# Kernel optimization log

Measured on AMD Instinct MI355X. Metric: run time of the kernel, lower is better.

Reference implementation:

```python
import jax, jax.numpy as jnp
import numpy as np

HEADS = 16
NU = 1
EPS = 1e-6


def dpfp(k):
    """Deterministic Parameter-Free Projection, normalized. k: [..., d_k] -> [..., 2*d_k*NU]."""
    x = jax.nn.relu(jnp.concatenate([k, -k], axis=-1))  # [..., 2*d_k]
    x_rolled = jnp.concatenate([jnp.roll(x, i, axis=-1) for i in range(1, NU + 1)], axis=-1)
    x_repeat = jnp.concatenate([x] * NU, axis=-1)
    phi = x_repeat * x_rolled
    return phi / (jnp.sum(phi, axis=-1, keepdims=True) + EPS)


def setup_inputs() -> dict:
    key = jax.random.key(0)
    ks = jax.random.split(key, 7)
    S, B, D, H = 4096, 4, 1024, HEADS
    scale = 0.02
    return {
        "x": jax.random.normal(ks[0], (S, B, D), dtype=jnp.float32),
        "Wq": jax.random.normal(ks[1], (D, D), dtype=jnp.float32) * scale,
        "Wk": jax.random.normal(ks[2], (D, D), dtype=jnp.float32) * scale,
        "Wv": jax.random.normal(ks[3], (D, D), dtype=jnp.float32) * scale,
        "Wb": jax.random.normal(ks[4], (D, H), dtype=jnp.float32) * scale,
        "Wo": jax.random.normal(ks[5], (D, D), dtype=jnp.float32) * scale,
        "bo": jnp.zeros((D,), dtype=jnp.float32),
    }


def reference(x, Wq, Wk, Wv, Wb, Wo, bo):
    S, B, D = x.shape
    H = HEADS
    dk = D // H
    d_dot = 2 * dk * NU

    # Projections: [S, B, H, d_k] (bias-free linears + head split)
    q = dpfp((x @ Wq).reshape(S, B, H, dk))   # [S, B, H, d_dot]
    k = dpfp((x @ Wk).reshape(S, B, H, dk))   # [S, B, H, d_dot]
    v = (x @ Wv).reshape(S, B, H, dk)          # [S, B, H, d_k]
    beta = jax.nn.sigmoid(x @ Wb).reshape(S, B, H, 1)  # [S, B, H, 1]

    W0 = jnp.zeros((B, H, dk, d_dot), dtype=x.dtype)  # fast-weight state

    def step(W, inputs):
        k_i, v_i, q_i, b_i = inputs  # [B,H,d_dot], [B,H,dk], [B,H,d_dot], [B,H,1]
        v_bar = jnp.einsum('bhvk,bhk->bhv', W, k_i)
        W = W + jnp.einsum('bhv,bhk->bhvk', b_i * (v_i - v_bar), k_i)
        y = jnp.einsum('bhvk,bhk->bhv', W, q_i)  # [B, H, dk]
        return W, y.reshape(B, H * dk)

    _, outputs = jax.lax.scan(step, W0, (k, v, q, beta))  # [S, B, D]
    return outputs @ Wo + bo
```

## Files before the change

kernel.cpp:

```cpp
#include <hip/hip_runtime.h>

#define S_LEN 4096
#define BATCH 4
#define NROWS 16384
#define DIM   1024
#define CHUNK 32
#define NCHUNK (S_LEN / CHUNK)

typedef __attribute__((ext_vector_type(8))) short short8;
typedef __attribute__((ext_vector_type(4))) float floatx4;
typedef _Float16 half_t;
typedef __attribute__((ext_vector_type(8))) _Float16 half8;

__device__ __forceinline__ float bf2f(short s) {
    union { unsigned int u; float f; } c;
    c.u = ((unsigned int)(unsigned short)s) << 16;
    return c.f;
}
__device__ __forceinline__ short f2bf(float f) {
    union { float f; unsigned int u; } c; c.f = f;
    unsigned int r = c.u + 0x7fffu + ((c.u >> 16) & 1u);
    return (short)(r >> 16);
}
__device__ __forceinline__ void split_bf16(float x, short& hi, short& lo) {
    short h = f2bf(x);
    hi = h;
    lo = f2bf(x - bf2f(h));
}

__device__ __forceinline__ float row16_allreduce(float x) {
    union fi { float f; int i; };
    fi a, b;
    a.f = x;
    b.i = __builtin_amdgcn_update_dpp(0, a.i, 0xB1,  0xF, 0xF, true); a.f += b.f;
    b.i = __builtin_amdgcn_update_dpp(0, a.i, 0x4E,  0xF, 0xF, true); a.f += b.f;
    b.i = __builtin_amdgcn_update_dpp(0, a.i, 0x124, 0xF, 0xF, true); a.f += b.f;
    b.i = __builtin_amdgcn_update_dpp(0, a.i, 0x128, 0xF, 0xF, true); a.f += b.f;
    return a.f;
}

__global__ __launch_bounds__(256) void transpose_k(const float* __restrict__ W,
                                                   float* __restrict__ Wt,
                                                   int K, int N) {
    int idx = blockIdx.x * 256 + threadIdx.x;
    if (idx >= N * K) return;
    int n = idx / K;
    int k = idx - n * K;
    Wt[idx] = W[k * N + n];
}

template <typename AT, int MODE>
__global__ __launch_bounds__(256) void gemm_bt(const AT* __restrict__ A,
                                               const float* __restrict__ Bt,
                                               void* __restrict__ Cout,
                                               const float* __restrict__ bias,
                                               int N, int K) {
    __shared__ __align__(16) short As_h[64][40], As_l[64][40];
    __shared__ __align__(16) short Bs_h[64][40], Bs_l[64][40];
    const int tid  = threadIdx.x;
    const int wave = tid >> 6, lane = tid & 63;
    const int row0 = blockIdx.x * 64, col0 = blockIdx.y * 64;
    const int lr = tid >> 2, lc = (tid & 3) * 8;
    const AT*    Ap = A  + (size_t)(row0 + lr) * K + lc;
    const float* Bp = Bt + (size_t)(col0 + lr) * K + lc;
    const int am = wave * 16 + (lane & 15);
    const int ak = (lane >> 4) * 8;
    floatx4 acc[4];
    #pragma unroll
    for (int t = 0; t < 4; ++t) acc[t] = (floatx4){0.f, 0.f, 0.f, 0.f};

    for (int k0 = 0; k0 < K; k0 += 32) {
        float av[8], bv[8];
        if constexpr (sizeof(AT) == 4) {
            floatx4 a0 = *(const floatx4*)(Ap + k0);
            floatx4 a1 = *(const floatx4*)(Ap + k0 + 4);
            #pragma unroll
            for (int j = 0; j < 4; ++j) { av[j] = a0[j]; av[4 + j] = a1[j]; }
        } else {
            half8 a = *(const half8*)(Ap + k0);
            #pragma unroll
            for (int j = 0; j < 8; ++j) av[j] = (float)a[j];
        }
        floatx4 b0 = *(const floatx4*)(Bp + k0);
        floatx4 b1 = *(const floatx4*)(Bp + k0 + 4);
        #pragma unroll
        for (int j = 0; j < 4; ++j) { bv[j] = b0[j]; bv[4 + j] = b1[j]; }

        short8 ah, al, bh, bl;
        #pragma unroll
        for (int j = 0; j < 8; ++j) {
            short h, l;
            split_bf16(av[j], h, l); ah[j] = h; al[j] = l;
            split_bf16(bv[j], h, l); bh[j] = h; bl[j] = l;
        }
        *(short8*)&As_h[lr][lc] = ah;
        *(short8*)&As_l[lr][lc] = al;
        *(short8*)&Bs_h[lr][lc] = bh;
        *(short8*)&Bs_l[lr][lc] = bl;
        __syncthreads();
        short8 afh = *(const short8*)&As_h[am][ak];
        short8 afl = *(const short8*)&As_l[am][ak];
        #pragma unroll
        for (int t = 0; t < 4; ++t) {
            short8 bfh = *(const short8*)&Bs_h[t * 16 + (lane & 15)][ak];
            short8 bfl = *(const short8*)&Bs_l[t * 16 + (lane & 15)][ak];
            acc[t] = __builtin_amdgcn_mfma_f32_16x16x32_bf16(afh, bfh, acc[t], 0, 0, 0);
            acc[t] = __builtin_amdgcn_mfma_f32_16x16x32_bf16(afh, bfl, acc[t], 0, 0, 0);
            acc[t] = __builtin_amdgcn_mfma_f32_16x16x32_bf16(afl, bfh, acc[t], 0, 0, 0);
        }
        __syncthreads();
    }
    const int crow = row0 + wave * 16 + (lane >> 4) * 4;
    const int ccol = lane & 15;
    #pragma unroll
    for (int t = 0; t < 4; ++t) {
        int col = col0 + t * 16 + ccol;
        #pragma unroll
        for (int r = 0; r < 4; ++r) {
            int row = crow + r;
            float v = acc[t][r];
            if (MODE == 0) {
                float b = bias ? bias[col] : 0.f;
                ((float*)Cout)[(size_t)row * N + col] = v + b;
            } else {
                ((half_t*)Cout)[(size_t)row * 2048 + (col >> 6) * 128 + (col & 63)] = (half_t)v;
            }
        }
    }
}

__global__ __launch_bounds__(256) void beta_kernel(const float* __restrict__ X,
                                                   const float* __restrict__ Wbt,
                                                   float* __restrict__ Beta) {
    int wid  = (blockIdx.x * 256 + threadIdx.x) >> 6;
    int lane = threadIdx.x & 63;
    if (wid >= NROWS) return;
    const float* xr = X + (size_t)wid * DIM + lane * 16;
    float xv[16];
    #pragma unroll
    for (int j = 0; j < 4; ++j) {
        floatx4 v = *(const floatx4*)(xr + j * 4);
        #pragma unroll
        for (int e = 0; e < 4; ++e) xv[j * 4 + e] = v[e];
    }
    #pragma unroll 1
    for (int h = 0; h < 16; ++h) {
        const float* wr = Wbt + h * DIM + lane * 16;
        float s = 0.f;
        #pragma unroll
        for (int j = 0; j < 4; ++j) {
            floatx4 v = *(const floatx4*)(wr + j * 4);
            #pragma unroll
            for (int e = 0; e < 4; ++e) s = fmaf(xv[j * 4 + e], v[e], s);
        }
        #pragma unroll
        for (int off = 32; off; off >>= 1) s += __shfl_xor(s, off);
        if (lane == 0) Beta[wid * 16 + h] = 1.f / (1.f + __expf(-s));
    }
}

__global__ __launch_bounds__(256) void dpfp_h(half_t* __restrict__ P) {
    int gw   = (blockIdx.x * 256 + threadIdx.x) >> 6;
    int lane = threadIdx.x & 63;
    half_t* base = P + (size_t)gw * 128;
    float p  = (float)base[lane];
    float pm = __shfl(p, (lane + 63) & 63);
    float rp  = fmaxf(p, 0.f),  rn  = fmaxf(-p, 0.f);
    float rpm = fmaxf(pm, 0.f), rnm = fmaxf(-pm, 0.f);
    float aprev = (lane == 0) ? rnm : rpm;
    float bprev = (lane == 0) ? rpm : rnm;
    float phi_a = rp * aprev;
    float phi_b = rn * bprev;
    float s = phi_a + phi_b;
    #pragma unroll
    for (int off = 32; off; off >>= 1) s += __shfl_xor(s, off);
    float inv = 1.f / (s + 1e-6f);
    base[lane]      = (half_t)(phi_a * inv);
    base[64 + lane] = (half_t)(phi_b * inv);
}


#define LOADSTEP(DK, DQ, STEP)                                              \
    {                                                                       \
        floatx4 _ka = *(const floatx4*)&Ks[bufi][STEP][tc * 8];             \
        floatx4 _kb = *(const floatx4*)&Ks[bufi][STEP][tc * 8 + 4];         \
        floatx4 _qa = *(const floatx4*)&Qs[bufi][STEP][tc * 8];             \
        floatx4 _qb = *(const floatx4*)&Qs[bufi][STEP][tc * 8 + 4];         \
        for (int _i = 0; _i < 4; ++_i) {                                    \
            DK[_i] = _ka[_i]; DK[4 + _i] = _kb[_i];                         \
            DQ[_i] = _qa[_i]; DQ[4 + _i] = _qb[_i];                         \
        }                                                                   \
    }

#define DOT8(RES, X, Y)                                                     \
    {                                                                       \
        float _s0 = X[0] * Y[0], _s1 = X[1] * Y[1];                         \
        _s0 = fmaf(X[2], Y[2], _s0); _s1 = fmaf(X[3], Y[3], _s1);           \
        _s0 = fmaf(X[4], Y[4], _s0); _s1 = fmaf(X[5], Y[5], _s1);           \
        _s0 = fmaf(X[6], Y[6], _s0); _s1 = fmaf(X[7], Y[7], _s1);           \
        RES = _s0 + _s1;                                                    \
    }

#define PAIR(CEK, CEQ, COK, COQ, CEV, CEB, COV, COB, CG,                    \
             NEK, NEQ, NOK, NOQ, NEV, NEB, NOV, NOB, NG, P)                 \
    {                                                                       \
        if ((P) + 1 < 16) {                                                 \
            LOADSTEP(NEK, NEQ, 2 * (P) + 2);                                \
            LOADSTEP(NOK, NOQ, 2 * (P) + 3);                                \
            NEV = Vs[bufi][2 * (P) + 2][row_l];                             \
            NEB = Bs[bufi][2 * (P) + 2];                                    \
            NOV = Vs[bufi][2 * (P) + 3][row_l];                             \
            NOB = Bs[bufi][2 * (P) + 3];                                    \
            NG  = *(const floatx4*)&GramLDS[(P) + 1][0];                    \
        }                                                                   \
        float _e0, _e1, _f0, _f1;                                           \
        DOT8(_e0, w, CEK); DOT8(_e1, w, COK);                               \
        DOT8(_f0, w, CEQ); DOT8(_f1, w, COQ);                               \
        _e0 = row16_allreduce(_e0); _e1 = row16_allreduce(_e1);             \
        _f0 = row16_allreduce(_f0); _f1 = row16_allreduce(_f1);             \
        float _c0 = CEB * (CEV - _e0);                                      \
        float _d1 = fmaf(_c0, CG[0], _e1);                                  \
        float _c1 = COB * (COV - _d1);                                      \
        float _y0 = fmaf(_c0, CG[1], _f0);                                  \
        float _y1 = fmaf(_c1, CG[3], fmaf(_c0, CG[2], _f1));                \
        for (int _j = 0; _j < 8; ++_j)                                      \
            w[_j] = fmaf(_c1, COK[_j], fmaf(_c0, CEK[_j], w[_j]));          \
        if (tc == 0) {                                                      \
            ybase[(size_t)((cc * CHUNK + 2 * (P))     * BATCH + b) * 1024] = (half_t)_y0; \
            ybase[(size_t)((cc * CHUNK + 2 * (P) + 1) * BATCH + b) * 1024] = (half_t)_y1; \
        }                                                                   \
    }

__global__ __launch_bounds__(256, 1) void scan_kernel(const half_t* __restrict__ PhiK,
                                                      const half_t* __restrict__ PhiQ,
                                                      const float* __restrict__ V,
                                                      const float* __restrict__ Beta,
                                                      half_t* __restrict__ Y) {
    __shared__ float Ks[2][CHUNK][128];
    __shared__ float Qs[2][CHUNK][128];
    __shared__ float Vs[2][CHUNK][16];
    __shared__ float Bs[2][CHUNK];
    __shared__ float GramLDS[16][4];

    const int bh = blockIdx.x >> 2;
    const int rc = blockIdx.x & 3;
    const int b = bh >> 4, h = bh & 15;
    const int tid = threadIdx.x;
    const int row_l = tid >> 4;
    const int tc = tid & 15;
    const int vrow = rc * 16 + row_l;

    const half_t* kg = PhiK + h * 128;
    const half_t* qg = PhiQ + h * 128;
    const float*  vg = V + h * 64 + rc * 16;
    const float*  bg = Beta + h;
    half_t* ybase = Y + h * 64 + vrow;

    {
        #pragma unroll
        for (int rpt = 0; rpt < 2; ++rpt) {
            int i = rpt * 256 + tid;
            int st = i >> 4, seg = i & 15, row = i & 15;
            size_t r = (size_t)(st * BATCH + b);
            half8 kv = *(const half8*)(kg + r * 2048 + seg * 8);
            half8 qv = *(const half8*)(qg + r * 2048 + seg * 8);
            floatx4 klo, khi, qlo, qhi;
            #pragma unroll
            for (int j = 0; j < 4; ++j) {
                klo[j] = (float)kv[j]; khi[j] = (float)kv[4 + j];
                qlo[j] = (float)qv[j]; qhi[j] = (float)qv[4 + j];
            }
            *(floatx4*)&Ks[0][st][seg * 8]     = klo;
            *(floatx4*)&Ks[0][st][seg * 8 + 4] = khi;
            *(floatx4*)&Qs[0][st][seg * 8]     = qlo;
            *(floatx4*)&Qs[0][st][seg * 8 + 4] = qhi;
            Vs[0][st][row] = vg[r * 1024 + row];
        }
        if (tid < CHUNK) {
            size_t r = (size_t)(tid * BATCH + b);
            Bs[0][tid] = bg[r * 16];
        }
    }
    __syncthreads();

    float w[8];
    #pragma unroll
    for (int j = 0; j < 8; ++j) w[j] = 0.f;

    for (int cc = 0; cc < NCHUNK; ++cc) {
        const int bufi = cc & 1;
        const bool more = (cc + 1 < NCHUNK);

        {
            float ka[8], kb[8], qa[8], qb[8];
            LOADSTEP(ka, qa, 2 * row_l);
            LOADSTEP(kb, qb, 2 * row_l + 1);
            float skk, s00, s01, s11;
            DOT8(skk, ka, kb);
            DOT8(s00, ka, qa);
            DOT8(s01, ka, qb);
            DOT8(s11, kb, qb);
            skk = row16_allreduce(skk);
            s00 = row16_allreduce(s00);
            s01 = row16_allreduce(s01);
            s11 = row16_allreduce(s11);
            if (tc == 0) {
                GramLDS[row_l][0] = skk;
                GramLDS[row_l][1] = s00;
                GramLDS[row_l][2] = s01;
                GramLDS[row_l][3] = s11;
            }
        }
        __syncthreads();

        half8 pk[2], pq[2];
        float pv[2], pb = 0.f;
        if (more) {
            #pragma unroll
            for (int rpt = 0; rpt < 2; ++rpt) {
                int i = rpt * 256 + tid;
                int st = i >> 4, seg = i & 15, row = i & 15;
                size_t r = (size_t)(((cc + 1) * CHUNK + st) * BATCH + b);
                pk[rpt] = *(const half8*)(kg + r * 2048 + seg * 8);
                pq[rpt] = *(const half8*)(qg + r * 2048 + seg * 8);
                pv[rpt] = vg[r * 1024 + row];
            }
            if (tid < CHUNK) {
                size_t r = (size_t)(((cc + 1) * CHUNK + tid) * BATCH + b);
                pb = bg[r * 16];
            }
        }

        float EK0[8], EQ0[8], OK0[8], OQ0[8];
        float EK1[8], EQ1[8], OK1[8], OQ1[8];
        float Ev0, Eb0, Ov0, Ob0, Ev1, Eb1, Ov1, Ob1;
        floatx4 G0, G1;
        LOADSTEP(EK0, EQ0, 0);
        LOADSTEP(OK0, OQ0, 1);
        Ev0 = Vs[bufi][0][row_l]; Eb0 = Bs[bufi][0];
        Ov0 = Vs[bufi][1][row_l]; Ob0 = Bs[bufi][1];
        G0 = *(const floatx4*)&GramLDS[0][0];

        #pragma unroll 1
        for (int p2 = 0; p2 < 16; p2 += 2) {
            PAIR(EK0, EQ0, OK0, OQ0, Ev0, Eb0, Ov0, Ob0, G0,
                 EK1, EQ1, OK1, OQ1, Ev1, Eb1, Ov1, Ob1, G1, p2);
            PAIR(EK1, EQ1, OK1, OQ1, Ev1, Eb1, Ov1, Ob1, G1,
                 EK0, EQ0, OK0, OQ0, Ev0, Eb0, Ov0, Ob0, G0, p2 + 1);
        }

        if (more) {
            const int bufn = bufi ^ 1;
            #pragma unroll
            for (int rpt = 0; rpt < 2; ++rpt) {
                int i = rpt * 256 + tid;
                int st = i >> 4, seg = i & 15, row = i & 15;
                floatx4 klo, khi, qlo, qhi;
                #pragma unroll
                for (int j = 0; j < 4; ++j) {
                    klo[j] = (float)pk[rpt][j]; khi[j] = (float)pk[rpt][4 + j];
                    qlo[j] = (float)pq[rpt][j]; qhi[j] = (float)pq[rpt][4 + j];
                }
                *(floatx4*)&Ks[bufn][st][seg * 8]     = klo;
                *(floatx4*)&Ks[bufn][st][seg * 8 + 4] = khi;
                *(floatx4*)&Qs[bufn][st][seg * 8]     = qlo;
                *(floatx4*)&Qs[bufn][st][seg * 8 + 4] = qhi;
                Vs[bufn][st][row] = pv[rpt];
            }
            if (tid < CHUNK) Bs[bufn][tid] = pb;
        }
        __syncthreads();
    }
}

extern "C" void kernel_launch(void* const* d_in, const int* in_sizes, int n_in,
                              void* d_out, int out_size, void* d_ws, size_t ws_size,
                              hipStream_t stream) {
    const float* x  = (const float*)d_in[0];
    const float* Wq = (const float*)d_in[1];
    const float* Wk = (const float*)d_in[2];
    const float* Wv = (const float*)d_in[3];
    const float* Wb = (const float*)d_in[4];
    const float* Wo = (const float*)d_in[5];
    const float* bo = (const float*)d_in[6];

    char* ws = (char*)d_ws;
    size_t off = 0;
    auto alloc = [&](size_t bytes) -> void* {
        void* p = ws + off;
        off += (bytes + 255) & ~(size_t)255;
        return p;
    };
    half_t* PhiQ = (half_t*)alloc((size_t)NROWS * 2048 * 2);
    half_t* PhiK = (half_t*)alloc((size_t)NROWS * 2048 * 2);
    half_t* Yb   = (half_t*)alloc((size_t)NROWS * 1024 * 2);
    float*  Beta = (float*)alloc((size_t)NROWS * 16 * 4);
    float*  Wqt  = (float*)alloc((size_t)1024 * 1024 * 4);
    float*  Wkt  = (float*)alloc((size_t)1024 * 1024 * 4);
    float*  Wvt  = (float*)alloc((size_t)1024 * 1024 * 4);
    float*  Wot  = (float*)alloc((size_t)1024 * 1024 * 4);
    float*  Wbt  = (float*)alloc((size_t)16 * 1024 * 4);
    float*  Vb   = (float*)d_out;

    transpose_k<<<4096, 256, 0, stream>>>(Wq, Wqt, 1024, 1024);
    transpose_k<<<4096, 256, 0, stream>>>(Wk, Wkt, 1024, 1024);
    transpose_k<<<4096, 256, 0, stream>>>(Wv, Wvt, 1024, 1024);
    transpose_k<<<4096, 256, 0, stream>>>(Wo, Wot, 1024, 1024);
    transpose_k<<<64,   256, 0, stream>>>(Wb, Wbt, 1024, 16);

    dim3 ggrid(NROWS / 64, DIM / 64);
    const int dgrid = (NROWS * 16) / 4;
    gemm_bt<float, 1><<<ggrid, 256, 0, stream>>>(x, Wqt, PhiQ, nullptr, DIM, DIM);
    dpfp_h<<<dgrid, 256, 0, stream>>>(PhiQ);
    gemm_bt<float, 1><<<ggrid, 256, 0, stream>>>(x, Wkt, PhiK, nullptr, DIM, DIM);
    dpfp_h<<<dgrid, 256, 0, stream>>>(PhiK);
    gemm_bt<float, 0><<<ggrid, 256, 0, stream>>>(x, Wvt, Vb, nullptr, DIM, DIM);
    beta_kernel<<<NROWS / 4, 256, 0, stream>>>(x, Wbt, Beta);
    scan_kernel<<<256, 256, 0, stream>>>(PhiK, PhiQ, Vb, Beta, Yb);
    gemm_bt<half_t, 0><<<ggrid, 256, 0, stream>>>(Yb, Wot, d_out, bo, DIM, DIM);
}
```

Baseline: 1.556 ms.

## Process four delta-rule steps per group using a 4x4 Gram block

Extends the blocked delta-rule recurrence from pairs of timesteps to groups of four. Each group needs the pairwise K·K and K·Q products, which are precomputed per chunk into a 16-entry Gram table. This halves the number of serialized W-dot/allreduce rounds per chunk. In exchange it adds more Gram computation, raises register pressure from holding four K/Q vectors per buffer, and has only half of the rows doing the Gram work.

```diff
diff --git a/kernel.cpp b/kernel.cpp
--- a/kernel.cpp
+++ b/kernel.cpp
@@ -180,16 +180,26 @@
 }
 
 
-#define LOADSTEP(DK, DQ, STEP)                                              \
+#define LOADK(DK, STEP)                                                     \
     {                                                                       \
-        floatx4 _ka = *(const floatx4*)&Ks[bufi][STEP][tc * 8];             \
-        floatx4 _kb = *(const floatx4*)&Ks[bufi][STEP][tc * 8 + 4];         \
-        floatx4 _qa = *(const floatx4*)&Qs[bufi][STEP][tc * 8];             \
-        floatx4 _qb = *(const floatx4*)&Qs[bufi][STEP][tc * 8 + 4];         \
-        for (int _i = 0; _i < 4; ++_i) {                                    \
-            DK[_i] = _ka[_i]; DK[4 + _i] = _kb[_i];                         \
-            DQ[_i] = _qa[_i]; DQ[4 + _i] = _qb[_i];                         \
-        }                                                                   \
+        floatx4 _a = *(const floatx4*)&Ks[bufi][(STEP)][tc * 8];            \
+        floatx4 _b = *(const floatx4*)&Ks[bufi][(STEP)][tc * 8 + 4];        \
+        for (int _i = 0; _i < 4; ++_i) { DK[_i] = _a[_i]; DK[4 + _i] = _b[_i]; } \
+    }
+
+#define LOADQ(DQ, STEP)                                                     \
+    {                                                                       \
+        floatx4 _a = *(const floatx4*)&Qs[bufi][(STEP)][tc * 8];            \
+        floatx4 _b = *(const floatx4*)&Qs[bufi][(STEP)][tc * 8 + 4];        \
+        for (int _i = 0; _i < 4; ++_i) { DQ[_i] = _a[_i]; DQ[4 + _i] = _b[_i]; } \
+    }
+
+#define LOADG(DG, QD)                                                       \
+    {                                                                       \
+        *(floatx4*)&DG[0]  = *(const floatx4*)&GramLDS[(QD)][0];            \
+        *(floatx4*)&DG[4]  = *(const floatx4*)&GramLDS[(QD)][4];            \
+        *(floatx4*)&DG[8]  = *(const floatx4*)&GramLDS[(QD)][8];            \
+        *(floatx4*)&DG[12] = *(const floatx4*)&GramLDS[(QD)][12];           \
     }
 
 #define DOT8(RES, X, Y)                                                     \
@@ -201,33 +211,51 @@
         RES = _s0 + _s1;                                                    \
     }
 
-#define PAIR(CEK, CEQ, COK, COQ, CEV, CEB, COV, COB, CG,                    \
-             NEK, NEQ, NOK, NOQ, NEV, NEB, NOV, NOB, NG, P)                 \
+#define QUAD(CK0, CK1, CK2, CK3, NK0, NK1, NK2, NK3, CG, NG, CV, CB, NV, NB, P) \
     {                                                                       \
-        if ((P) + 1 < 16) {                                                 \
-            LOADSTEP(NEK, NEQ, 2 * (P) + 2);                                \
-            LOADSTEP(NOK, NOQ, 2 * (P) + 3);                                \
-            NEV = Vs[bufi][2 * (P) + 2][row_l];                             \
-            NEB = Bs[bufi][2 * (P) + 2];                                    \
-            NOV = Vs[bufi][2 * (P) + 3][row_l];                             \
-            NOB = Bs[bufi][2 * (P) + 3];                                    \
-            NG  = *(const floatx4*)&GramLDS[(P) + 1][0];                    \
+        float _e0, _e1, _e2, _e3, _f0, _f1, _f2, _f3;                       \
+        DOT8(_e0, w, CK0); DOT8(_e1, w, CK1);                               \
+        DOT8(_e2, w, CK2); DOT8(_e3, w, CK3);                               \
+        DOT8(_f0, w, QQ0); DOT8(_f1, w, QQ1);                               \
+        DOT8(_f2, w, QQ2); DOT8(_f3, w, QQ3);                               \
+        if ((P) + 1 < 8) {                                                  \
+            LOADQ(QQ0, 4 * (P) + 4); LOADQ(QQ1, 4 * (P) + 5);               \
+            LOADQ(QQ2, 4 * (P) + 6); LOADQ(QQ3, 4 * (P) + 7);               \
+            LOADK(NK0, 4 * (P) + 4); LOADK(NK1, 4 * (P) + 5);               \
+            LOADK(NK2, 4 * (P) + 6); LOADK(NK3, 4 * (P) + 7);               \
+            NV[0] = Vs[bufi][4 * (P) + 4][row_l];                           \
+            NV[1] = Vs[bufi][4 * (P) + 5][row_l];                           \
+            NV[2] = Vs[bufi][4 * (P) + 6][row_l];                           \
+            NV[3] = Vs[bufi][4 * (P) + 7][row_l];                           \
+            NB[0] = Bs[bufi][4 * (P) + 4];                                  \
+            NB[1] = Bs[bufi][4 * (P) + 5];                                  \
+            NB[2] = Bs[bufi][4 * (P) + 6];                                  \
+            NB[3] = Bs[bufi][4 * (P) + 7];                                  \
+            LOADG(NG, (P) + 1);                                             \
         }                                                                   \
-        float _e0, _e1, _f0, _f1;                                           \
-        DOT8(_e0, w, CEK); DOT8(_e1, w, COK);                               \
-        DOT8(_f0, w, CEQ); DOT8(_f1, w, COQ);                               \
         _e0 = row16_allreduce(_e0); _e1 = row16_allreduce(_e1);             \
+        _e2 = row16_allreduce(_e2); _e3 = row16_allreduce(_e3);             \
         _f0 = row16_allreduce(_f0); _f1 = row16_allreduce(_f1);             \
-        float _c0 = CEB * (CEV - _e0);                                      \
+        _f2 = row16_allreduce(_f2); _f3 = row16_allreduce(_f3);             \
+        float _c0 = CB[0] * (CV[0] - _e0);                                  \
         float _d1 = fmaf(_c0, CG[0], _e1);                                  \
-        float _c1 = COB * (COV - _d1);                                      \
-        float _y0 = fmaf(_c0, CG[1], _f0);                                  \
-        float _y1 = fmaf(_c1, CG[3], fmaf(_c0, CG[2], _f1));                \
+        float _c1 = CB[1] * (CV[1] - _d1);                                  \
+        float _d2 = fmaf(_c1, CG[3], fmaf(_c0, CG[1], _e2));                \
+        float _c2 = CB[2] * (CV[2] - _d2);                                  \
+        float _d3 = fmaf(_c2, CG[5], fmaf(_c1, CG[4], fmaf(_c0, CG[2], _e3))); \
+        float _c3 = CB[3] * (CV[3] - _d3);                                  \
+        float _y0 = fmaf(_c0, CG[6], _f0);                                  \
+        float _y1 = fmaf(_c1, CG[10], fmaf(_c0, CG[7], _f1));               \
+        float _y2 = fmaf(_c2, CG[13], fmaf(_c1, CG[11], fmaf(_c0, CG[8], _f2))); \
+        float _y3 = fmaf(_c3, CG[15], fmaf(_c2, CG[14], fmaf(_c1, CG[12], fmaf(_c0, CG[9], _f3)))); \
         for (int _j = 0; _j < 8; ++_j)                                      \
-            w[_j] = fmaf(_c1, COK[_j], fmaf(_c0, CEK[_j], w[_j]));          \
+            w[_j] = fmaf(_c3, CK3[_j], fmaf(_c2, CK2[_j],                   \
+                    fmaf(_c1, CK1[_j], fmaf(_c0, CK0[_j], w[_j]))));        \
         if (tc == 0) {                                                      \
-            ybase[(size_t)((cc * CHUNK + 2 * (P))     * BATCH + b) * 1024] = (half_t)_y0; \
-            ybase[(size_t)((cc * CHUNK + 2 * (P) + 1) * BATCH + b) * 1024] = (half_t)_y1; \
+            ybase[(size_t)((cc * CHUNK + 4 * (P))     * BATCH + b) * 1024] = (half_t)_y0; \
+            ybase[(size_t)((cc * CHUNK + 4 * (P) + 1) * BATCH + b) * 1024] = (half_t)_y1; \
+            ybase[(size_t)((cc * CHUNK + 4 * (P) + 2) * BATCH + b) * 1024] = (half_t)_y2; \
+            ybase[(size_t)((cc * CHUNK + 4 * (P) + 3) * BATCH + b) * 1024] = (half_t)_y3; \
         }                                                                   \
     }
 
@@ -240,7 +268,7 @@
     __shared__ float Qs[2][CHUNK][128];
     __shared__ float Vs[2][CHUNK][16];
     __shared__ float Bs[2][CHUNK];
-    __shared__ float GramLDS[16][4];
+    __shared__ __align__(16) float GramLDS[8][16];
 
     const int bh = blockIdx.x >> 2;
     const int rc = blockIdx.x & 3;
@@ -291,28 +319,6 @@
         const int bufi = cc & 1;
         const bool more = (cc + 1 < NCHUNK);
 
-        {
-            float ka[8], kb[8], qa[8], qb[8];
-            LOADSTEP(ka, qa, 2 * row_l);
-            LOADSTEP(kb, qb, 2 * row_l + 1);
-            float skk, s00, s01, s11;
-            DOT8(skk, ka, kb);
-            DOT8(s00, ka, qa);
-            DOT8(s01, ka, qb);
-            DOT8(s11, kb, qb);
-            skk = row16_allreduce(skk);
-            s00 = row16_allreduce(s00);
-            s01 = row16_allreduce(s01);
-            s11 = row16_allreduce(s11);
-            if (tc == 0) {
-                GramLDS[row_l][0] = skk;
-                GramLDS[row_l][1] = s00;
-                GramLDS[row_l][2] = s01;
-                GramLDS[row_l][3] = s11;
-            }
-        }
-        __syncthreads();
-
         half8 pk[2], pq[2];
         float pv[2], pb = 0.f;
         if (more) {
@@ -331,22 +337,46 @@
             }
         }
 
-        float EK0[8], EQ0[8], OK0[8], OQ0[8];
-        float EK1[8], EQ1[8], OK1[8], OQ1[8];
-        float Ev0, Eb0, Ov0, Ob0, Ev1, Eb1, Ov1, Ob1;
-        floatx4 G0, G1;
-        LOADSTEP(EK0, EQ0, 0);
-        LOADSTEP(OK0, OQ0, 1);
-        Ev0 = Vs[bufi][0][row_l]; Eb0 = Bs[bufi][0];
-        Ov0 = Vs[bufi][1][row_l]; Ob0 = Bs[bufi][1];
-        G0 = *(const floatx4*)&GramLDS[0][0];
+        {
+            const int qd = row_l & 7;
+            float k0[8], k1[8], k2[8], k3[8], q0[8], q1[8], q2[8], q3[8];
+            LOADK(k0, 4 * qd);     LOADK(k1, 4 * qd + 1);
+            LOADK(k2, 4 * qd + 2); LOADK(k3, 4 * qd + 3);
+            LOADQ(q0, 4 * qd);     LOADQ(q1, 4 * qd + 1);
+            LOADQ(q2, 4 * qd + 2); LOADQ(q3, 4 * qd + 3);
+            float g[16];
+            DOT8(g[0],  k0, k1); DOT8(g[1],  k0, k2); DOT8(g[2],  k0, k3);
+            DOT8(g[3],  k1, k2); DOT8(g[4],  k1, k3); DOT8(g[5],  k2, k3);
+            DOT8(g[6],  k0, q0); DOT8(g[7],  k0, q1); DOT8(g[8],  k0, q2);
+            DOT8(g[9],  k0, q3); DOT8(g[10], k1, q1); DOT8(g[11], k1, q2);
+            DOT8(g[12], k1, q3); DOT8(g[13], k2, q2); DOT8(g[14], k2, q3);
+            DOT8(g[15], k3, q3);
+            #pragma unroll
+            for (int i = 0; i < 16; ++i) g[i] = row16_allreduce(g[i]);
+            if (tc == 0 && row_l < 8) {
+                #pragma unroll
+                for (int i = 0; i < 16; ++i) GramLDS[qd][i] = g[i];
+            }
+        }
+        __syncthreads();
+
+        float KA0[8], KA1[8], KA2[8], KA3[8];
+        float KB0[8], KB1[8], KB2[8], KB3[8];
+        float QQ0[8], QQ1[8], QQ2[8], QQ3[8];
+        float GA[16], GB[16];
+        float vA[4], vB[4], bA[4], bB[4];
+        LOADK(KA0, 0); LOADK(KA1, 1); LOADK(KA2, 2); LOADK(KA3, 3);
+        LOADQ(QQ0, 0); LOADQ(QQ1, 1); LOADQ(QQ2, 2); LOADQ(QQ3, 3);
+        vA[0] = Vs[bufi][0][row_l]; vA[1] = Vs[bufi][1][row_l];
+        vA[2] = Vs[bufi][2][row_l]; vA[3] = Vs[bufi][3][row_l];
+        bA[0] = Bs[bufi][0]; bA[1] = Bs[bufi][1];
+        bA[2] = Bs[bufi][2]; bA[3] = Bs[bufi][3];
+        LOADG(GA, 0);
 
         #pragma unroll 1
-        for (int p2 = 0; p2 < 16; p2 += 2) {
-            PAIR(EK0, EQ0, OK0, OQ0, Ev0, Eb0, Ov0, Ob0, G0,
-                 EK1, EQ1, OK1, OQ1, Ev1, Eb1, Ov1, Ob1, G1, p2);
-            PAIR(EK1, EQ1, OK1, OQ1, Ev1, Eb1, Ov1, Ob1, G1,
-                 EK0, EQ0, OK0, OQ0, Ev0, Eb0, Ov0, Ob0, G0, p2 + 1);
+        for (int p = 0; p < 8; p += 2) {
+            QUAD(KA0, KA1, KA2, KA3, KB0, KB1, KB2, KB3, GA, GB, vA, bA, vB, bB, p);
+            QUAD(KB0, KB1, KB2, KB3, KA0, KA1, KA2, KA3, GB, GA, vB, bB, vA, bA, p + 1);
         }
 
         if (more) {
```

New measurement: 1.704 ms. +9.5%, slower.
